# Kernel tuning notes

Measured on AMD Instinct MI355X. Metric: run time of the kernel, lower is better.

## Reference

```python
import jax, jax.numpy as jnp
import numpy as np

N_NODES = 100000
N_EDGES = 3200000
EPS = 1e-5
NEG_SLOPE = 0.1


def _glorot(key, fan_in, fan_out):
    lim = np.sqrt(6.0 / (fan_in + fan_out))
    return jax.random.uniform(key, (fan_in, fan_out), jnp.float32, -lim, lim)


def setup_inputs() -> dict:
    key = jax.random.key(0)
    ks = jax.random.split(key, 16)
    x = jax.random.normal(ks[0], (N_NODES, 3), jnp.float32)
    edge_index = jax.random.randint(ks[1], (2, N_EDGES), 0, N_NODES, jnp.int32)
    dims = [(3, 64), (64, 64), (64, 256), (256, 256), (256, 512), (512, 1)]
    inp = {"x": x, "edge_index": edge_index}
    for i, (fi, fo) in enumerate(dims):
        inp[f"W{i+1}"] = _glorot(ks[2 + i], fi, fo)
        inp[f"b{i+1}"] = jnp.zeros((fo,), jnp.float32)
    for i, fo in enumerate([64, 64, 256, 256, 512]):
        inp[f"g{i+1}"] = jnp.ones((fo,), jnp.float32)
        inp[f"bt{i+1}"] = jnp.zeros((fo,), jnp.float32)
    return inp


def _gcn_conv(h, W, b, src, dst, dis):
    # transform first (cheaper when out_dim <= in_dim is not guaranteed, but
    # avoids gathering raw features twice); then edge-normalized scatter-add.
    hw = h @ W                                   # [N, Fo]
    norm = dis[src] * dis[dst]                   # [E]
    agg = jax.ops.segment_sum(hw[src] * norm[:, None], dst, num_segments=N_NODES)
    agg = agg + (dis * dis)[:, None] * hw        # self-loop term (norm = dis_i^2)
    return agg + b


def _bn(h, g, bt):
    mu = jnp.mean(h, axis=0)
    var = jnp.mean((h - mu) ** 2, axis=0)        # biased var, as torch BN
    return (h - mu) * jax.lax.rsqrt(var + EPS) * g + bt


def _lrelu(h):
    return jnp.where(h > 0, h, NEG_SLOPE * h)


def reference(x, edge_index, W1, b1, W2, b2, W3, b3, W4, b4, W5, b5, W6, b6,
              g1, bt1, g2, bt2, g3, bt3, g4, bt4, g5, bt5):
    src, dst = edge_index[0], edge_index[1]
    # degree includes the added self-loop (+1), symmetric normalization
    deg = jax.ops.segment_sum(jnp.ones((N_EDGES,), x.dtype), dst,
                              num_segments=N_NODES) + 1.0
    dis = jax.lax.rsqrt(deg)

    h = x
    Ws = [W1, W2, W3, W4, W5]
    bs = [b1, b2, b3, b4, b5]
    gs = [g1, g2, g3, g4, g5]
    bts = [bt1, bt2, bt3, bt4, bt5]
    for W, b, g, bt in zip(Ws, bs, gs, bts):
        h = _gcn_conv(h, W, b, src, dst, dis)
        h = _lrelu(_bn(h, g, bt))
    h = _gcn_conv(h, W6, b6, src, dst, dis)
    return jax.nn.sigmoid(h)
```

## Files before the change

### kernel.cpp

```cpp
#include <hip/hip_runtime.h>
#include <math.h>

typedef unsigned short u16;
typedef unsigned int u32;
typedef __attribute__((ext_vector_type(8))) short bf16x8;
typedef __attribute__((ext_vector_type(4))) float f32x4;

constexpr float EPS_BN = 1e-5f;
constexpr float NEG = 0.1f;
constexpr int LDP = 800;

static inline int cdiv(int a, int b) { return (a + b - 1) / b; }


__device__ __forceinline__ float b2f_lo(u32 v) { return __uint_as_float(v << 16); }
__device__ __forceinline__ float b2f_hi(u32 v) { return __uint_as_float(v & 0xFFFF0000u); }
__device__ __forceinline__ float b2f(u16 v) { return __uint_as_float(((u32)v) << 16); }
__device__ __forceinline__ u16 f2b(float f) {
  u32 u = __float_as_uint(f);
  u32 r = u + 0x7FFFu + ((u >> 16) & 1u);
  return (u16)(r >> 16);
}
__device__ __forceinline__ u32 pack2(float a, float b) {
  return (u32)f2b(a) | ((u32)f2b(b) << 16);
}
__device__ __forceinline__ void unpack8(uint4 v, float* o) {
  o[0] = b2f_lo(v.x); o[1] = b2f_hi(v.x);
  o[2] = b2f_lo(v.y); o[3] = b2f_hi(v.y);
  o[4] = b2f_lo(v.z); o[5] = b2f_hi(v.z);
  o[6] = b2f_lo(v.w); o[7] = b2f_hi(v.w);
}
__device__ __forceinline__ void unpack4(uint2 v, float* o) {
  o[0] = b2f_lo(v.x); o[1] = b2f_hi(v.x);
  o[2] = b2f_lo(v.y); o[3] = b2f_hi(v.y);
}


__global__ void k_zero_i32(int* p, int n) {
  int i = blockIdx.x * blockDim.x + threadIdx.x;
  if (i < n) p[i] = 0;
}

__global__ __launch_bounds__(256) void k_bcount(const int* __restrict__ dst,
                                                int* __restrict__ bucketCnt, int E) {
  __shared__ int hist[256];
  int tid = threadIdx.x;
  hist[tid] = 0;
  __syncthreads();
  int e0 = blockIdx.x * 4096;
#pragma unroll
  for (int i = 0; i < 16; ++i) {
    int e = e0 + i * 256 + tid;
    if (e < E) atomicAdd(&hist[dst[e] >> 9], 1);
  }
  __syncthreads();
  int h = hist[tid];
  if (h > 0) atomicAdd(&bucketCnt[tid], h);
}

__global__ void k_bscan(const int* __restrict__ bucketCnt, int* __restrict__ bucketOff,
                        int* __restrict__ bucketCur, int NB, int E) {
  __shared__ int s[256];
  int tid = threadIdx.x;
  int v = (tid < NB) ? bucketCnt[tid] : 0;
  s[tid] = v;
  __syncthreads();
  for (int off = 1; off < 256; off <<= 1) {
    int t = (tid >= off) ? s[tid - off] : 0;
    __syncthreads();
    s[tid] += t;
    __syncthreads();
  }
  if (tid < NB) bucketOff[tid] = s[tid] - v;
  if (tid == NB) bucketOff[NB] = E;
  if (tid < NB) bucketCur[tid] = 0;
}

__global__ __launch_bounds__(256) void k_bucket(const int* __restrict__ src,
                                                const int* __restrict__ dst,
                                                const int* __restrict__ bucketOff,
                                                int* __restrict__ bucketCur,
                                                uint2* __restrict__ ebuf, int E) {
  __shared__ int hist[256];
  __shared__ int base[256];
  __shared__ int lcur[256];
  int tid = threadIdx.x;
  hist[tid] = 0; lcur[tid] = 0;
  __syncthreads();
  int e0 = blockIdx.x * 4096;
  int ss[16], dd[16];
#pragma unroll
  for (int i = 0; i < 16; ++i) {
    int e = e0 + i * 256 + tid;
    if (e < E) {
      ss[i] = src[e]; dd[i] = dst[e];
      atomicAdd(&hist[dd[i] >> 9], 1);
    } else dd[i] = -1;
  }
  __syncthreads();
  int h = hist[tid];
  if (h > 0) base[tid] = bucketOff[tid] + atomicAdd(&bucketCur[tid], h);
  __syncthreads();
#pragma unroll
  for (int i = 0; i < 16; ++i) {
    if (dd[i] >= 0) {
      int bk = dd[i] >> 9;
      int p = atomicAdd(&lcur[bk], 1);
      ebuf[base[bk] + p] = make_uint2((u32)ss[i], (u32)dd[i]);
    }
  }
}

__global__ __launch_bounds__(256) void k_csr(const uint2* __restrict__ ebuf,
                                             const int* __restrict__ bucketOff,
                                             int* __restrict__ rowoff,
                                             int* __restrict__ col,
                                             float* __restrict__ dis,
                                             int N, int E, int NB) {
  __shared__ int hist[512];
  __shared__ int loff[512];
  __shared__ int scan_s[256];
  int b = blockIdx.x;
  int tid = threadIdx.x;
  int ebase = bucketOff[b], eend = bucketOff[b + 1];
  int ecnt = eend - ebase;
  hist[tid] = 0; hist[tid + 256] = 0;
  __syncthreads();
  for (int i = tid; i < ecnt; i += 256)
    atomicAdd(&hist[ebuf[ebase + i].y & 511], 1);
  __syncthreads();
  int h0 = hist[2 * tid], h1 = hist[2 * tid + 1];
  int ts = h0 + h1;
  scan_s[tid] = ts;
  __syncthreads();
  for (int off = 1; off < 256; off <<= 1) {
    int t = (tid >= off) ? scan_s[tid - off] : 0;
    __syncthreads();
    scan_s[tid] += t;
    __syncthreads();
  }
  int excl = scan_s[tid] - ts;
  loff[2 * tid] = excl;
  loff[2 * tid + 1] = excl + h0;
  __syncthreads();
  int gbase = b * 512;
  for (int i = tid; i < 512; i += 256) {
    int node = gbase + i;
    if (node < N) {
      rowoff[node] = ebase + loff[i];
      dis[node] = rsqrtf((float)hist[i] + 1.0f);
    }
  }
  if (b == NB - 1 && tid == 0) rowoff[N] = E;
  __syncthreads();
  for (int i = tid; i < ecnt; i += 256) {
    uint2 ed = ebuf[ebase + i];
    int p = atomicAdd(&loff[ed.y & 511], 1);
    col[ebase + p] = (int)ed.x;
  }
}


__global__ void k_u1(const float* __restrict__ x, const float* __restrict__ dis,
                     u16* __restrict__ u, int n) {
  int i = blockIdx.x * blockDim.x + threadIdx.x;
  if (i >= n) return;
  float d = dis[i];
  u32 p0 = pack2(d * x[i * 3 + 0], d * x[i * 3 + 1]);
  u32 p1 = pack2(d * x[i * 3 + 2], 0.0f);
  ((uint2*)u)[i] = make_uint2(p0, p1);
}

__global__ void k_agg1(const u16* __restrict__ u, const int* __restrict__ rowoff,
                       const int* __restrict__ col, const float* __restrict__ dis,
                       u16* __restrict__ a, int n) {
  int wid = (blockIdx.x * blockDim.x + threadIdx.x) >> 6;
  int lane = threadIdx.x & 63;
  if (wid >= n) return;
  const uint2* u2 = (const uint2*)u;
  float a0 = 0.f, a1 = 0.f, a2 = 0.f;
  int beg = rowoff[wid], end = rowoff[wid + 1];
  for (int e = beg + lane; e < end; e += 64) {
    uint2 w = u2[col[e]];
    a0 += b2f_lo(w.x); a1 += b2f_hi(w.x); a2 += b2f_lo(w.y);
  }
#pragma unroll
  for (int off = 32; off; off >>= 1) {
    a0 += __shfl_xor(a0, off); a1 += __shfl_xor(a1, off); a2 += __shfl_xor(a2, off);
  }
  if (lane == 0) {
    uint2 s = u2[wid];
    a0 += b2f_lo(s.x); a1 += b2f_hi(s.x); a2 += b2f_lo(s.y);
    float d = dis[wid];
    ((uint2*)a)[wid] = make_uint2(pack2(d * a0, d * a1), pack2(d * a2, 0.0f));
  }
}

__global__ void k_gemm1(const u16* __restrict__ a, const float* __restrict__ W,
                        const float* __restrict__ b, u16* __restrict__ z, int n) {
  __shared__ float Ws[3][64];
  __shared__ float bs[64];
  int tid = threadIdx.x;
  if (tid < 192) Ws[tid / 64][tid % 64] = W[tid];
  if (tid < 64) bs[tid] = b[tid];
  __syncthreads();
  int f = tid % 64, r = tid / 64;
  int node = blockIdx.x * 4 + r;
  if (node >= n) return;
  uint2 v = ((const uint2*)a)[node];
  float a0 = b2f_lo(v.x), a1 = b2f_hi(v.x), a2 = b2f_lo(v.y);
  float zv = a0 * Ws[0][f] + a1 * Ws[1][f] + a2 * Ws[2][f] + bs[f];
  z[(size_t)node * 64 + f] = f2b(zv);
}


__global__ void k_agg64(const u16* __restrict__ u, const int* __restrict__ rowoff,
                        const int* __restrict__ col, const float* __restrict__ dis,
                        u16* __restrict__ a, int n) {
  int wid = (blockIdx.x * blockDim.x + threadIdx.x) >> 6;
  int lane = threadIdx.x & 63;
  if (wid >= n) return;
  int sub = lane >> 4, c = lane & 15;
  const uint2* u2 = (const uint2*)u;
  float acc[4] = {0.f, 0.f, 0.f, 0.f};
  if (sub == 0) {
    float s[4]; unpack4(u2[(size_t)wid * 16 + c], s);
#pragma unroll
    for (int k = 0; k < 4; ++k) acc[k] = s[k];
  }
  int beg = rowoff[wid], end = rowoff[wid + 1];
  int e = beg + sub;
  for (; e + 4 < end; e += 8) {
    int j1 = col[e], j2 = col[e + 4];
    uint2 v1 = u2[(size_t)j1 * 16 + c];
    uint2 v2 = u2[(size_t)j2 * 16 + c];
    float f1[4], f2[4];
    unpack4(v1, f1); unpack4(v2, f2);
#pragma unroll
    for (int k = 0; k < 4; ++k) acc[k] += f1[k] + f2[k];
  }
  if (e < end) {
    float f1[4]; unpack4(u2[(size_t)col[e] * 16 + c], f1);
#pragma unroll
    for (int k = 0; k < 4; ++k) acc[k] += f1[k];
  }
#pragma unroll
  for (int k = 0; k < 4; ++k) {
    acc[k] += __shfl_xor(acc[k], 16);
    acc[k] += __shfl_xor(acc[k], 32);
  }
  if (sub == 0) {
    float d = dis[wid];
    ((uint2*)a)[(size_t)wid * 16 + c] =
        make_uint2(pack2(d * acc[0], d * acc[1]), pack2(d * acc[2], d * acc[3]));
  }
}

__global__ void k_agg256(const u16* __restrict__ u, const int* __restrict__ rowoff,
                         const int* __restrict__ col, const float* __restrict__ dis,
                         u16* __restrict__ a, int n) {
  int wid = (blockIdx.x * blockDim.x + threadIdx.x) >> 6;
  int lane = threadIdx.x & 63;
  if (wid >= n) return;
  int sub = lane >> 5, c = lane & 31;
  const uint4* u4 = (const uint4*)u;
  float acc[8] = {0.f, 0.f, 0.f, 0.f, 0.f, 0.f, 0.f, 0.f};
  if (sub == 0) {
    float s[8]; unpack8(u4[(size_t)wid * 32 + c], s);
#pragma unroll
    for (int k = 0; k < 8; ++k) acc[k] = s[k];
  }
  int beg = rowoff[wid], end = rowoff[wid + 1];
  int e = beg + sub;
  for (; e + 2 < end; e += 4) {
    int j1 = col[e], j2 = col[e + 2];
    uint4 v1 = u4[(size_t)j1 * 32 + c];
    uint4 v2 = u4[(size_t)j2 * 32 + c];
    float f1[8], f2[8];
    unpack8(v1, f1); unpack8(v2, f2);
#pragma unroll
    for (int k = 0; k < 8; ++k) acc[k] += f1[k] + f2[k];
  }
  if (e < end) {
    float f1[8]; unpack8(u4[(size_t)col[e] * 32 + c], f1);
#pragma unroll
    for (int k = 0; k < 8; ++k) acc[k] += f1[k];
  }
#pragma unroll
  for (int k = 0; k < 8; ++k) acc[k] += __shfl_xor(acc[k], 32);
  if (sub == 0) {
    float d = dis[wid];
    uint4 r;
    r.x = pack2(d * acc[0], d * acc[1]);
    r.y = pack2(d * acc[2], d * acc[3]);
    r.z = pack2(d * acc[4], d * acc[5]);
    r.w = pack2(d * acc[6], d * acc[7]);
    ((uint4*)a)[(size_t)wid * 32 + c] = r;
  }
}


__global__ void k_u(u16* __restrict__ z, const float* __restrict__ scaleF,
                    const float* __restrict__ shiftF, const float* __restrict__ dis,
                    int n, int lg) {
  size_t idx = (size_t)blockIdx.x * blockDim.x + threadIdx.x;
  size_t tot = ((size_t)n) << lg;
  if (idx >= tot) return;
  int g = (int)(idx & ((1u << lg) - 1));
  int node = (int)(idx >> lg);
  uint4 v = ((const uint4*)z)[idx];
  float f[8];
  unpack8(v, f);
  int f0 = g * 8;
  float4 s0 = *(const float4*)&scaleF[f0];
  float4 s1 = *(const float4*)&scaleF[f0 + 4];
  float4 h0 = *(const float4*)&shiftF[f0];
  float4 h1 = *(const float4*)&shiftF[f0 + 4];
  float d = dis[node];
  float o[8];
  o[0] = f[0] * s0.x + h0.x; o[1] = f[1] * s0.y + h0.y;
  o[2] = f[2] * s0.z + h0.z; o[3] = f[3] * s0.w + h0.w;
  o[4] = f[4] * s1.x + h1.x; o[5] = f[5] * s1.y + h1.y;
  o[6] = f[6] * s1.z + h1.z; o[7] = f[7] * s1.w + h1.w;
#pragma unroll
  for (int k = 0; k < 8; ++k) {
    float a = o[k];
    a = (a > 0.f) ? a : NEG * a;
    o[k] = d * a;
  }
  uint4 r;
  r.x = pack2(o[0], o[1]); r.y = pack2(o[2], o[3]);
  r.z = pack2(o[4], o[5]); r.w = pack2(o[6], o[7]);
  ((uint4*)z)[idx] = r;
}


__global__ void k_wt(const float* __restrict__ W, u16* __restrict__ WT, int K, int Fo) {
  int i = blockIdx.x * blockDim.x + threadIdx.x;
  if (i >= K * Fo) return;
  int f = i / K, k = i - f * K;
  WT[i] = f2b(W[(size_t)k * Fo + f]);
}

__global__ __launch_bounds__(256) void k_gemm(const u16* __restrict__ A,
                                              const u16* __restrict__ WT,
                                              const float* __restrict__ bias,
                                              u16* __restrict__ C,
                                              float* __restrict__ psum,
                                              float* __restrict__ psq,
                                              int n, int K, int Fo, int nby) {
  __shared__ u16 As[128][72];
  __shared__ u16 Bs[128][72];
  int tid = threadIdx.x;
  int nwg = gridDim.x;
  int bid = blockIdx.x;
  int q = nwg >> 3, rr = nwg & 7;
  int xcd = bid & 7, pos = bid >> 3;
  int wgid = (xcd < rr ? xcd * (q + 1) : rr * (q + 1) + (xcd - rr) * q) + pos;
  int bx = wgid / nby, by = wgid - bx * nby;
  int bm0 = bx * 128, bn0 = by * 128;
  int lane = tid & 63, wid = tid >> 6;
  int wm = wid >> 1, wn = wid & 1;
  int lr = tid & 127;
  int lh = (tid >> 7) * 32;
  int fr = lane & 15, fg = lane >> 4;
  f32x4 acc[4][4];
#pragma unroll
  for (int i = 0; i < 4; ++i)
#pragma unroll
    for (int j = 0; j < 4; ++j) acc[i][j] = (f32x4)0.0f;

  for (int kt = 0; kt < K; kt += 64) {
    {
      int row = bm0 + lr;
      uint4 v[4];
#pragma unroll
      for (int i = 0; i < 4; ++i) {
        v[i] = make_uint4(0u, 0u, 0u, 0u);
        if (row < n) v[i] = *(const uint4*)&A[(size_t)row * K + kt + lh + i * 8];
      }
      int fo = bn0 + lr;
      uint4 w[4];
#pragma unroll
      for (int i = 0; i < 4; ++i) {
        w[i] = make_uint4(0u, 0u, 0u, 0u);
        if (fo < Fo) w[i] = *(const uint4*)&WT[(size_t)fo * K + kt + lh + i * 8];
      }
#pragma unroll
      for (int i = 0; i < 4; ++i) *(uint4*)&As[lr][lh + i * 8] = v[i];
#pragma unroll
      for (int i = 0; i < 4; ++i) *(uint4*)&Bs[lr][lh + i * 8] = w[i];
    }
    __syncthreads();
#pragma unroll
    for (int ks = 0; ks < 2; ++ks) {
      int k0 = ks * 32 + fg * 8;
      bf16x8 af[4], bf[4];
#pragma unroll
      for (int mi = 0; mi < 4; ++mi) af[mi] = *(const bf16x8*)&As[wm * 64 + mi * 16 + fr][k0];
#pragma unroll
      for (int ni = 0; ni < 4; ++ni) bf[ni] = *(const bf16x8*)&Bs[wn * 64 + ni * 16 + fr][k0];
#pragma unroll
      for (int mi = 0; mi < 4; ++mi)
#pragma unroll
        for (int ni = 0; ni < 4; ++ni)
          acc[mi][ni] = __builtin_amdgcn_mfma_f32_16x16x32_bf16(af[mi], bf[ni], acc[mi][ni], 0, 0, 0);
    }
    __syncthreads();
  }
  float* s2 = (float*)&As[0][0];
#pragma unroll
  for (int ni = 0; ni < 4; ++ni) {
    int gc = bn0 + wn * 64 + ni * 16 + fr;
    float ps = 0.f, pq = 0.f;
    if (gc < Fo) {
      float bv = bias[gc];
#pragma unroll
      for (int mi = 0; mi < 4; ++mi) {
#pragma unroll
        for (int rg = 0; rg < 4; ++rg) {
          int gr = bm0 + wm * 64 + mi * 16 + fg * 4 + rg;
          if (gr < n) {
            float v = acc[mi][ni][rg] + bv;
            C[(size_t)gr * Fo + gc] = f2b(v);
            ps += v; pq += v * v;
          }
        }
      }
    }
    ps += __shfl_xor(ps, 16); ps += __shfl_xor(ps, 32);
    pq += __shfl_xor(pq, 16); pq += __shfl_xor(pq, 32);
    if (fg == 0 && gc < Fo) {
      int cl = wn * 64 + ni * 16 + fr;
      s2[wm * 128 + cl] = ps;
      s2[256 + wm * 128 + cl] = pq;
    }
  }
  __syncthreads();
  if (tid < 128) {
    int gc = bn0 + tid;
    if (gc < Fo) {
      psum[(size_t)gc * LDP + bx] = s2[tid] + s2[128 + tid];
      psq[(size_t)gc * LDP + bx] = s2[256 + tid] + s2[384 + tid];
    }
  }
}


__global__ void k_colred(const u16* __restrict__ z, int Fo, int n, int rowsPerChunk,
                         float* __restrict__ psum, float* __restrict__ psq) {
  int fl = threadIdx.x & 63;
  int rg = threadIdx.x >> 6;
  int f = blockIdx.y * 64 + fl;
  int r0 = blockIdx.x * rowsPerChunk;
  int r1 = min(n, r0 + rowsPerChunk);
  float s = 0.f, sq = 0.f;
  for (int r = r0 + rg; r < r1; r += 4) {
    float v = b2f(z[(size_t)r * Fo + f]);
    s += v;
    sq += v * v;
  }
  __shared__ float ls[4][64], lq[4][64];
  ls[rg][fl] = s; lq[rg][fl] = sq;
  __syncthreads();
  if (rg == 0) {
    psum[(size_t)f * LDP + blockIdx.x] = ls[0][fl] + ls[1][fl] + ls[2][fl] + ls[3][fl];
    psq[(size_t)f * LDP + blockIdx.x] = lq[0][fl] + lq[1][fl] + lq[2][fl] + lq[3][fl];
  }
}

__global__ void k_bnparams(const float* __restrict__ psum, const float* __restrict__ psq,
                           int Fo, int nChunks, int n,
                           const float* __restrict__ g, const float* __restrict__ bt,
                           float* __restrict__ scaleF, float* __restrict__ shiftF) {
  int f = blockIdx.x * 4 + (threadIdx.x >> 6);
  int lane = threadIdx.x & 63;
  if (f >= Fo) return;
  float s = 0.f, sq = 0.f;
  const float* ps = &psum[(size_t)f * LDP];
  const float* pq = &psq[(size_t)f * LDP];
  for (int c = lane; c < nChunks; c += 64) { s += ps[c]; sq += pq[c]; }
#pragma unroll
  for (int off = 32; off; off >>= 1) {
    s += __shfl_xor(s, off);
    sq += __shfl_xor(sq, off);
  }
  if (lane == 0) {
    float inv = 1.0f / (float)n;
    float mu = s * inv;
    float var = sq * inv - mu * mu;
    float rs = rsqrtf(var + EPS_BN) * g[f];
    scaleF[f] = rs;
    shiftF[f] = bt[f] - mu * rs;
  }
}


__global__ void k_dot512(const u16* __restrict__ z, const float* __restrict__ scaleF,
                         const float* __restrict__ shiftF, const float* __restrict__ w6,
                         const float* __restrict__ dis, float* __restrict__ v, int n) {
  __shared__ float ws[512], scs[512], shs[512];
  int tid = threadIdx.x;
  for (int i = tid; i < 512; i += 256) { ws[i] = w6[i]; scs[i] = scaleF[i]; shs[i] = shiftF[i]; }
  __syncthreads();
  int lane = tid % 64, wv = tid / 64;
  int node = blockIdx.x * 4 + wv;
  if (node >= n) return;
  uint4 vz = *(const uint4*)&z[(size_t)node * 512 + lane * 8];
  float f[8];
  unpack8(vz, f);
  int f0 = lane * 8;
  float s = 0.f;
#pragma unroll
  for (int k = 0; k < 8; ++k) {
    float a = f[k] * scs[f0 + k] + shs[f0 + k];
    a = (a > 0.f) ? a : NEG * a;
    s += a * ws[f0 + k];
  }
#pragma unroll
  for (int off = 32; off > 0; off >>= 1) s += __shfl_down(s, off);
  if (lane == 0) v[node] = dis[node] * s;
}

__global__ void k_final(const float* __restrict__ v, const int* __restrict__ rowoff,
                        const int* __restrict__ col, const float* __restrict__ dis,
                        const float* __restrict__ b6, float* __restrict__ out, int n) {
  int wid = (blockIdx.x * blockDim.x + threadIdx.x) >> 6;
  int lane = threadIdx.x & 63;
  if (wid >= n) return;
  float acc = 0.f;
  int beg = rowoff[wid], end = rowoff[wid + 1];
  for (int e = beg + lane; e < end; e += 64) acc += v[col[e]];
#pragma unroll
  for (int off = 32; off; off >>= 1) acc += __shfl_xor(acc, off);
  if (lane == 0) {
    float zz = dis[wid] * (acc + v[wid]) + b6[0];
    out[wid] = 1.0f / (1.0f + expf(-zz));
  }
}


extern "C" void kernel_launch(void* const* d_in, const int* in_sizes, int n_in,
                              void* d_out, int out_size, void* d_ws, size_t ws_size,
                              hipStream_t stream) {
  const float* x = (const float*)d_in[0];
  const int* ei = (const int*)d_in[1];
  const int N = in_sizes[0] / 3;
  const int E = in_sizes[1] / 2;
  const int* srcIdx = ei;
  const int* dstIdx = ei + E;

  const float* W[6]; const float* b[6];
  for (int i = 0; i < 6; ++i) { W[i] = (const float*)d_in[2 + 2 * i]; b[i] = (const float*)d_in[3 + 2 * i]; }
  const float* g[5]; const float* bt[5];
  for (int i = 0; i < 5; ++i) { g[i] = (const float*)d_in[14 + 2 * i]; bt[i] = (const float*)d_in[15 + 2 * i]; }

  char* wsB = (char*)d_ws;
  size_t off = 0;
  auto alloc = [&](size_t bytes) -> void* {
    void* p = wsB + off;
    off = (off + bytes + 255) & ~(size_t)255;
    return p;
  };

  const int NB = cdiv(N, 512);
  int* rowoff = (int*)alloc((size_t)(N + 1) * 4);
  int* col = (int*)alloc((size_t)E * 4);
  float* dis = (float*)alloc((size_t)N * 4);
  float* vbuf = (float*)alloc((size_t)N * 4);
  float* scaleF = (float*)alloc(512 * 4);
  float* shiftF = (float*)alloc(512 * 4);
  u16* WTb = (u16*)alloc((size_t)512 * 256 * 2);
  int* bucketCnt = (int*)alloc(256 * 4);
  int* bucketOff = (int*)alloc(257 * 4);
  int* bucketCur = (int*)alloc(256 * 4);
  const int nbx = cdiv(N, 128);
  float* psum = (float*)alloc((size_t)512 * LDP * 4);
  float* psq = (float*)alloc((size_t)512 * LDP * 4);
  u16* Zb = (u16*)alloc((size_t)N * 512 * 2);
  u16* Ab = (u16*)alloc((size_t)N * 256 * 2);
  uint2* ebuf = (uint2*)Ab;

  const int EB = cdiv(E, 4096);
  k_zero_i32<<<1, 256, 0, stream>>>(bucketCnt, 256);
  k_bcount<<<EB, 256, 0, stream>>>(dstIdx, bucketCnt, E);
  k_bscan<<<1, 256, 0, stream>>>(bucketCnt, bucketOff, bucketCur, NB, E);
  k_bucket<<<EB, 256, 0, stream>>>(srcIdx, dstIdx, bucketOff, bucketCur, ebuf, E);
  k_csr<<<NB, 256, 0, stream>>>(ebuf, bucketOff, rowoff, col, dis, N, E, NB);

  auto gemm = [&](const u16* Ain, int layer, int K, int Fo, u16* Cout) {
    k_wt<<<cdiv(K * Fo, 256), 256, 0, stream>>>(W[layer], WTb, K, Fo);
    int nby = cdiv(Fo, 128);
    k_gemm<<<nbx * nby, 256, 0, stream>>>(Ain, WTb, b[layer], Cout, psum, psq, N, K, Fo, nby);
    k_bnparams<<<cdiv(Fo, 4), 256, 0, stream>>>(psum, psq, Fo, nbx, N,
                                                g[layer], bt[layer], scaleF, shiftF);
  };

  const int waveGrid = cdiv(N * 64, 256);

  k_u1<<<cdiv(N, 256), 256, 0, stream>>>(x, dis, Zb, N);
  k_agg1<<<waveGrid, 256, 0, stream>>>(Zb, rowoff, col, dis, Ab, N);
  k_gemm1<<<cdiv(N, 4), 256, 0, stream>>>(Ab, W[0], b[0], Zb, N);
  {
    const int rowsPerChunk = 2048;
    const int nChunks = cdiv(N, rowsPerChunk);
    dim3 grid(nChunks, 1);
    k_colred<<<grid, 256, 0, stream>>>(Zb, 64, N, rowsPerChunk, psum, psq);
    k_bnparams<<<cdiv(64, 4), 256, 0, stream>>>(psum, psq, 64, nChunks, N, g[0], bt[0], scaleF, shiftF);
  }

  k_u<<<cdiv(N * 8, 256), 256, 0, stream>>>(Zb, scaleF, shiftF, dis, N, 3);
  k_agg64<<<waveGrid, 256, 0, stream>>>(Zb, rowoff, col, dis, Ab, N);
  gemm(Ab, 1, 64, 64, Zb);

  k_u<<<cdiv(N * 8, 256), 256, 0, stream>>>(Zb, scaleF, shiftF, dis, N, 3);
  k_agg64<<<waveGrid, 256, 0, stream>>>(Zb, rowoff, col, dis, Ab, N);
  gemm(Ab, 2, 64, 256, Zb);

  k_u<<<cdiv(N * 32, 256), 256, 0, stream>>>(Zb, scaleF, shiftF, dis, N, 5);
  k_agg256<<<waveGrid, 256, 0, stream>>>(Zb, rowoff, col, dis, Ab, N);
  gemm(Ab, 3, 256, 256, Zb);

  k_u<<<cdiv(N * 32, 256), 256, 0, stream>>>(Zb, scaleF, shiftF, dis, N, 5);
  k_agg256<<<waveGrid, 256, 0, stream>>>(Zb, rowoff, col, dis, Ab, N);
  gemm(Ab, 4, 256, 512, Zb);

  k_dot512<<<cdiv(N, 4), 256, 0, stream>>>(Zb, scaleF, shiftF, W[5], dis, vbuf, N);
  k_final<<<waveGrid, 256, 0, stream>>>(vbuf, rowoff, col, dis, b[5], (float*)d_out, N);
}
```

Measured before the change: 1.246 ms.

## Fuse layer-1 kernels, pack edge buffer, prefetch indices, batch weight transposes

Merges the layer-1 prescale, aggregation and 3->64 transform into one kernel that gathers fp32 x and dis directly, removing two launches and intermediate buffers. Packs each bucketed edge into a single 32-bit word (src<<9 | local dst), halving edge-buffer traffic during CSR build, which assumes node indices fit in 23 bits. Restructures the 64- and 256-wide aggregation loops to prefetch the next column indices before the current gathers, and converts all weight transposes in one upfront launch.

```diff
diff --git a/kernel.cpp b/kernel.cpp
--- a/kernel.cpp
+++ b/kernel.cpp
@@ -80,7 +80,7 @@
                                                 const int* __restrict__ dst,
                                                 const int* __restrict__ bucketOff,
                                                 int* __restrict__ bucketCur,
-                                                uint2* __restrict__ ebuf, int E) {
+                                                u32* __restrict__ ebuf, int E) {
   __shared__ int hist[256];
   __shared__ int base[256];
   __shared__ int lcur[256];
@@ -106,12 +106,12 @@
     if (dd[i] >= 0) {
       int bk = dd[i] >> 9;
       int p = atomicAdd(&lcur[bk], 1);
-      ebuf[base[bk] + p] = make_uint2((u32)ss[i], (u32)dd[i]);
-    }
-  }
-}
-
-__global__ __launch_bounds__(256) void k_csr(const uint2* __restrict__ ebuf,
+      ebuf[base[bk] + p] = ((u32)ss[i] << 9) | ((u32)dd[i] & 511u);
+    }
+  }
+}
+
+__global__ __launch_bounds__(256) void k_csr(const u32* __restrict__ ebuf,
                                              const int* __restrict__ bucketOff,
                                              int* __restrict__ rowoff,
                                              int* __restrict__ col,
@@ -127,7 +127,7 @@
   hist[tid] = 0; hist[tid + 256] = 0;
   __syncthreads();
   for (int i = tid; i < ecnt; i += 256)
-    atomicAdd(&hist[ebuf[ebase + i].y & 511], 1);
+    atomicAdd(&hist[ebuf[ebase + i] & 511u], 1);
   __syncthreads();
   int h0 = hist[2 * tid], h1 = hist[2 * tid + 1];
   int ts = h0 + h1;
@@ -154,63 +154,39 @@
   if (b == NB - 1 && tid == 0) rowoff[N] = E;
   __syncthreads();
   for (int i = tid; i < ecnt; i += 256) {
-    uint2 ed = ebuf[ebase + i];
-    int p = atomicAdd(&loff[ed.y & 511], 1);
-    col[ebase + p] = (int)ed.x;
-  }
-}
-
-
-__global__ void k_u1(const float* __restrict__ x, const float* __restrict__ dis,
-                     u16* __restrict__ u, int n) {
-  int i = blockIdx.x * blockDim.x + threadIdx.x;
-  if (i >= n) return;
-  float d = dis[i];
-  u32 p0 = pack2(d * x[i * 3 + 0], d * x[i * 3 + 1]);
-  u32 p1 = pack2(d * x[i * 3 + 2], 0.0f);
-  ((uint2*)u)[i] = make_uint2(p0, p1);
-}
-
-__global__ void k_agg1(const u16* __restrict__ u, const int* __restrict__ rowoff,
-                       const int* __restrict__ col, const float* __restrict__ dis,
-                       u16* __restrict__ a, int n) {
+    u32 ed = ebuf[ebase + i];
+    int p = atomicAdd(&loff[ed & 511u], 1);
+    col[ebase + p] = (int)(ed >> 9);
+  }
+}
+
+
+__global__ void k_l1(const float* __restrict__ x, const int* __restrict__ rowoff,
+                     const int* __restrict__ col, const float* __restrict__ dis,
+                     const float* __restrict__ W, const float* __restrict__ b,
+                     u16* __restrict__ z, int n) {
   int wid = (blockIdx.x * blockDim.x + threadIdx.x) >> 6;
   int lane = threadIdx.x & 63;
   if (wid >= n) return;
-  const uint2* u2 = (const uint2*)u;
   float a0 = 0.f, a1 = 0.f, a2 = 0.f;
   int beg = rowoff[wid], end = rowoff[wid + 1];
   for (int e = beg + lane; e < end; e += 64) {
-    uint2 w = u2[col[e]];
-    a0 += b2f_lo(w.x); a1 += b2f_hi(w.x); a2 += b2f_lo(w.y);
+    int j = col[e];
+    float dj = dis[j];
+    a0 += dj * x[j * 3 + 0];
+    a1 += dj * x[j * 3 + 1];
+    a2 += dj * x[j * 3 + 2];
   }
 #pragma unroll
   for (int off = 32; off; off >>= 1) {
     a0 += __shfl_xor(a0, off); a1 += __shfl_xor(a1, off); a2 += __shfl_xor(a2, off);
   }
-  if (lane == 0) {
-    uint2 s = u2[wid];
-    a0 += b2f_lo(s.x); a1 += b2f_hi(s.x); a2 += b2f_lo(s.y);
-    float d = dis[wid];
-    ((uint2*)a)[wid] = make_uint2(pack2(d * a0, d * a1), pack2(d * a2, 0.0f));
-  }
-}
-
-__global__ void k_gemm1(const u16* __restrict__ a, const float* __restrict__ W,
-                        const float* __restrict__ b, u16* __restrict__ z, int n) {
-  __shared__ float Ws[3][64];
-  __shared__ float bs[64];
-  int tid = threadIdx.x;
-  if (tid < 192) Ws[tid / 64][tid % 64] = W[tid];
-  if (tid < 64) bs[tid] = b[tid];
-  __syncthreads();
-  int f = tid % 64, r = tid / 64;
-  int node = blockIdx.x * 4 + r;
-  if (node >= n) return;
-  uint2 v = ((const uint2*)a)[node];
-  float a0 = b2f_lo(v.x), a1 = b2f_hi(v.x), a2 = b2f_lo(v.y);
-  float zv = a0 * Ws[0][f] + a1 * Ws[1][f] + a2 * Ws[2][f] + bs[f];
-  z[(size_t)node * 64 + f] = f2b(zv);
+  float di = dis[wid];
+  a0 = di * (a0 + di * x[wid * 3 + 0]);
+  a1 = di * (a1 + di * x[wid * 3 + 1]);
+  a2 = di * (a2 + di * x[wid * 3 + 2]);
+  float zv = a0 * W[lane] + a1 * W[64 + lane] + a2 * W[128 + lane] + b[lane];
+  z[(size_t)wid * 64 + lane] = f2b(zv);
 }
 
 
@@ -230,19 +206,26 @@
   }
   int beg = rowoff[wid], end = rowoff[wid + 1];
   int e = beg + sub;
-  for (; e + 4 < end; e += 8) {
-    int j1 = col[e], j2 = col[e + 4];
-    uint2 v1 = u2[(size_t)j1 * 16 + c];
-    uint2 v2 = u2[(size_t)j2 * 16 + c];
-    float f1[4], f2[4];
-    unpack4(v1, f1); unpack4(v2, f2);
-#pragma unroll
-    for (int k = 0; k < 4; ++k) acc[k] += f1[k] + f2[k];
-  }
-  if (e < end) {
-    float f1[4]; unpack4(u2[(size_t)col[e] * 16 + c], f1);
-#pragma unroll
-    for (int k = 0; k < 4; ++k) acc[k] += f1[k];
+  int j1 = (e < end) ? col[e] : -1;
+  int j2 = (e + 4 < end) ? col[e + 4] : -1;
+  while (j1 >= 0) {
+    int en = e + 8;
+    int nj1 = -1, nj2 = -1;
+    if (j2 >= 0) {
+      if (en < end) nj1 = col[en];
+      if (en + 4 < end) nj2 = col[en + 4];
+    }
+    {
+      float f1[4]; unpack4(u2[(size_t)j1 * 16 + c], f1);
+#pragma unroll
+      for (int k = 0; k < 4; ++k) acc[k] += f1[k];
+    }
+    if (j2 >= 0) {
+      float f2[4]; unpack4(u2[(size_t)j2 * 16 + c], f2);
+#pragma unroll
+      for (int k = 0; k < 4; ++k) acc[k] += f2[k];
+    }
+    e = en; j1 = nj1; j2 = nj2;
   }
 #pragma unroll
   for (int k = 0; k < 4; ++k) {
@@ -272,19 +255,26 @@
   }
   int beg = rowoff[wid], end = rowoff[wid + 1];
   int e = beg + sub;
-  for (; e + 2 < end; e += 4) {
-    int j1 = col[e], j2 = col[e + 2];
-    uint4 v1 = u4[(size_t)j1 * 32 + c];
-    uint4 v2 = u4[(size_t)j2 * 32 + c];
-    float f1[8], f2[8];
-    unpack8(v1, f1); unpack8(v2, f2);
-#pragma unroll
-    for (int k = 0; k < 8; ++k) acc[k] += f1[k] + f2[k];
-  }
-  if (e < end) {
-    float f1[8]; unpack8(u4[(size_t)col[e] * 32 + c], f1);
-#pragma unroll
-    for (int k = 0; k < 8; ++k) acc[k] += f1[k];
+  int j1 = (e < end) ? col[e] : -1;
+  int j2 = (e + 2 < end) ? col[e + 2] : -1;
+  while (j1 >= 0) {
+    int en = e + 4;
+    int nj1 = -1, nj2 = -1;
+    if (j2 >= 0) {
+      if (en < end) nj1 = col[en];
+      if (en + 2 < end) nj2 = col[en + 2];
+    }
+    {
+      float f1[8]; unpack8(u4[(size_t)j1 * 32 + c], f1);
+#pragma unroll
+      for (int k = 0; k < 8; ++k) acc[k] += f1[k];
+    }
+    if (j2 >= 0) {
+      float f2[8]; unpack8(u4[(size_t)j2 * 32 + c], f2);
+#pragma unroll
+      for (int k = 0; k < 8; ++k) acc[k] += f2[k];
+    }
+    e = en; j1 = nj1; j2 = nj2;
   }
 #pragma unroll
   for (int k = 0; k < 8; ++k) acc[k] += __shfl_xor(acc[k], 32);
@@ -335,12 +325,21 @@
 }
 
 
-__global__ void k_wt(const float* __restrict__ W, u16* __restrict__ WT, int K, int Fo) {
+__global__ void k_wt_all(const float* __restrict__ W2, const float* __restrict__ W3,
+                         const float* __restrict__ W4, const float* __restrict__ W5,
+                         u16* __restrict__ WT) {
   int i = blockIdx.x * blockDim.x + threadIdx.x;
-  if (i >= K * Fo) return;
-  int f = i / K, k = i - f * K;
+  const float* W; int K, Fo, base;
+  if (i < 4096)        { W = W2; K = 64;  Fo = 64;  base = 0; }
+  else if (i < 20480)  { W = W3; K = 64;  Fo = 256; base = 4096; }
+  else if (i < 86016)  { W = W4; K = 256; Fo = 256; base = 20480; }
+  else if (i < 217088) { W = W5; K = 256; Fo = 512; base = 86016; }
+  else return;
+  int idx = i - base;
+  int f = idx / K, k = idx - f * K;
   WT[i] = f2b(W[(size_t)k * Fo + f]);
 }
+
 
 __global__ __launch_bounds__(256) void k_gemm(const u16* __restrict__ A,
                                               const u16* __restrict__ WT,
@@ -570,7 +569,7 @@
   float* vbuf = (float*)alloc((size_t)N * 4);
   float* scaleF = (float*)alloc(512 * 4);
   float* shiftF = (float*)alloc(512 * 4);
-  u16* WTb = (u16*)alloc((size_t)512 * 256 * 2);
+  u16* WTb = (u16*)alloc((size_t)217088 * 2);
   int* bucketCnt = (int*)alloc(256 * 4);
   int* bucketOff = (int*)alloc(257 * 4);
   int* bucketCur = (int*)alloc(256 * 4);
@@ -579,7 +578,10 @@
   float* psq = (float*)alloc((size_t)512 * LDP * 4);
   u16* Zb = (u16*)alloc((size_t)N * 512 * 2);
   u16* Ab = (u16*)alloc((size_t)N * 256 * 2);
-  uint2* ebuf = (uint2*)Ab;
+  u32* ebuf = (u32*)Ab;
+
+  const int wtOff[5] = {0, 0, 4096, 20480, 86016};
+  k_wt_all<<<cdiv(217088, 256), 256, 0, stream>>>(W[1], W[2], W[3], W[4], WTb);
 
   const int EB = cdiv(E, 4096);
   k_zero_i32<<<1, 256, 0, stream>>>(bucketCnt, 256);
@@ -589,18 +591,16 @@
   k_csr<<<NB, 256, 0, stream>>>(ebuf, bucketOff, rowoff, col, dis, N, E, NB);
 
   auto gemm = [&](const u16* Ain, int layer, int K, int Fo, u16* Cout) {
-    k_wt<<<cdiv(K * Fo, 256), 256, 0, stream>>>(W[layer], WTb, K, Fo);
     int nby = cdiv(Fo, 128);
-    k_gemm<<<nbx * nby, 256, 0, stream>>>(Ain, WTb, b[layer], Cout, psum, psq, N, K, Fo, nby);
+    k_gemm<<<nbx * nby, 256, 0, stream>>>(Ain, WTb + wtOff[layer], b[layer], Cout,
+                                          psum, psq, N, K, Fo, nby);
     k_bnparams<<<cdiv(Fo, 4), 256, 0, stream>>>(psum, psq, Fo, nbx, N,
                                                 g[layer], bt[layer], scaleF, shiftF);
   };
 
   const int waveGrid = cdiv(N * 64, 256);
 
-  k_u1<<<cdiv(N, 256), 256, 0, stream>>>(x, dis, Zb, N);
-  k_agg1<<<waveGrid, 256, 0, stream>>>(Zb, rowoff, col, dis, Ab, N);
-  k_gemm1<<<cdiv(N, 4), 256, 0, stream>>>(Ab, W[0], b[0], Zb, N);
+  k_l1<<<waveGrid, 256, 0, stream>>>(x, rowoff, col, dis, W[0], b[0], Zb, N);
   {
     const int rowsPerChunk = 2048;
     const int nChunks = cdiv(N, rowsPerChunk);
```

Measured after the change: 1.235 ms. About the same (-0.8%).
